# Optimization experiments

Measured on AMD Instinct MI355X. Metric: run time of the kernel, lower is better.

The kernel has to match this reference:

```python
import jax, jax.numpy as jnp
import numpy as np

B, N, H, D, L = 4, 1024, 8, 256, 4
SVD, NSP = 16, 512
DK = D // H
EPS = 1e-6


def setup_inputs() -> dict:
    key = jax.random.key(0)
    ks = jax.random.split(key, 40)
    p = {}
    p["x"] = jax.random.normal(ks[0], (B, N, D), jnp.float32)
    p["in_degrees"] = jax.random.randint(ks[1], (N,), 0, N)
    p["out_degrees"] = jax.random.randint(ks[2], (N,), 0, N)
    p["spatial_pos"] = jax.random.randint(ks[3], (N, N), 0, NSP)
    p["svd_emb"] = jax.random.normal(ks[4], (N, 2 * SVD), jnp.float32)
    # embedding tables (padding_idx=0 -> zero row)
    p["in_deg_emb"] = (0.02 * jax.random.normal(ks[5], (N, D), jnp.float32)).at[0].set(0.0)
    p["out_deg_emb"] = (0.02 * jax.random.normal(ks[6], (N, D), jnp.float32)).at[0].set(0.0)
    p["spatial_emb"] = (0.02 * jax.random.normal(ks[7], (NSP, H), jnp.float32)).at[0].set(0.0)
    # SVD linear (stored [in, out]; y = x @ W + b)
    p["W_svd"] = 0.02 * jax.random.normal(ks[8], (2 * SVD, D), jnp.float32)
    p["b_svd"] = jnp.zeros((D,), jnp.float32)
    # per-layer stacked transformer params
    names = ["Wq", "Wk", "Wv", "Wa", "W1", "W2"]
    for i, nm in enumerate(names):
        p[nm] = 0.05 * jax.random.normal(ks[9 + i], (L, D, D), jnp.float32)
    for nm in ["bq", "bk", "bv", "ba", "b1", "b2", "ln1_b", "ln2_b"]:
        p[nm] = jnp.zeros((L, D), jnp.float32)
    p["ln1_g"] = jnp.ones((L, D), jnp.float32)
    p["ln2_g"] = jnp.ones((L, D), jnp.float32)
    return p


def _ln(x, g, b):
    mu = jnp.mean(x, axis=-1, keepdims=True)
    var = jnp.mean(jnp.square(x - mu), axis=-1, keepdims=True)
    return (x - mu) * jax.lax.rsqrt(var + EPS) * g + b


def _forward(x, svd_emb, W_svd, b_svd, in_deg_emb, out_deg_emb, spatial_emb,
             Wq, bq, Wk, bk, Wv, bv, Wa, ba, ln1_g, ln1_b,
             W1, b1, W2, b2, ln2_g, ln2_b,
             in_degrees, out_degrees, spatial_pos):
    # node-level: degree embeddings ([N,D] broadcasts over batch)
    x = x + in_deg_emb[in_degrees] + out_deg_emb[out_degrees]
    # node-level: SVD embedding (deterministic sign = +1 -> concat(u, -v))
    pos = jnp.concatenate([svd_emb[:, :SVD], -svd_emb[:, SVD:]], axis=-1)
    x = x + pos @ W_svd + b_svd
    # attention-level spatial bias: [N,N,H] -> [H,N,N], broadcast over batch
    attn_bias = jnp.transpose(spatial_emb[spatial_pos], (2, 0, 1))
    scale = 1.0 / jnp.sqrt(jnp.asarray(DK, x.dtype))

    def body(h, params):
        wq, bq_, wk, bk_, wv, bv_, wa, ba_, g1, b1_, w1, bb1, w2, bb2, g2, b2_ = params
        q = (h @ wq + bq_).reshape(B, N, H, DK)
        k = (h @ wk + bk_).reshape(B, N, H, DK)
        v = (h @ wv + bv_).reshape(B, N, H, DK)
        # scores [B,H,N,N] + spatial bias [H,N,N]
        scores = jnp.einsum('bqhd,bkhd->bhqk', q, k) * scale + attn_bias
        attn = jax.nn.softmax(scores, axis=-1)
        o = jnp.einsum('bhqk,bkhd->bqhd', attn, v).reshape(B, N, D)
        h = _ln(h + o @ wa + ba_, g1, b1_)
        f = jnp.maximum(h @ w1 + bb1, 0.0) @ w2 + bb2
        h = _ln(h + f, g2, b2_)
        return h, None

    x, _ = jax.lax.scan(body, x, (Wq, bq, Wk, bk, Wv, bv, Wa, ba, ln1_g, ln1_b,
                                  W1, b1, W2, b2, ln2_g, ln2_b))
    return x


def reference(x, svd_emb, W_svd, b_svd, in_deg_emb, out_deg_emb, spatial_emb,
              Wq, bq, Wk, bk, Wv, bv, Wa, ba, ln1_g, ln1_b,
              W1, b1, W2, b2, ln2_g, ln2_b,
              in_degrees, out_degrees, spatial_pos):
    return _forward(x, svd_emb, W_svd, b_svd, in_deg_emb, out_deg_emb, spatial_emb,
                    Wq, bq, Wk, bk, Wv, bv, Wa, ba, ln1_g, ln1_b,
                    W1, b1, W2, b2, ln2_g, ln2_b,
                    in_degrees, out_degrees, spatial_pos)
```

## Files before the change

### kernel.cpp

```cpp
#include <hip/hip_runtime.h>
#include <hip/hip_bf16.h>
#include <math.h>

#define NN 1024
#define BB 4
#define HH 8
#define DD 256
#define LL 4
#define DKK 32
#define MM 4096
#define EPSF 1e-6f
#define LOG2EF 1.4426950408889634f
#define SCLOG2E 0.2550348625f

typedef __attribute__((ext_vector_type(8))) short short8;
typedef __attribute__((ext_vector_type(4))) float f32x4;
typedef unsigned int u32;

__device__ __forceinline__ unsigned short f2bf(float f) {
    __hip_bfloat16 h = __float2bfloat16(f);
    return *(unsigned short*)&h;
}
__device__ __forceinline__ float bf2f(unsigned short u) {
    unsigned v = ((unsigned)u) << 16;
    return __builtin_bit_cast(float, v);
}

__global__ __launch_bounds__(256) void init_kernel(
    const float* __restrict__ x, const int* __restrict__ deg_in,
    const int* __restrict__ deg_out, const float* __restrict__ svd,
    const float* __restrict__ in_emb, const float* __restrict__ out_emb,
    const float* __restrict__ Wsvd, const float* __restrict__ bsvd,
    const float* __restrict__ Wq, const float* __restrict__ Wk,
    const float* __restrict__ Wv, const float* __restrict__ Wa,
    const float* __restrict__ W1, const float* __restrict__ W2,
    const int* __restrict__ sp, const float* __restrict__ spemb,
    float* __restrict__ h, short* __restrict__ hb,
    short* __restrict__ Wt, short* __restrict__ bsw)
{
    int blk = blockIdx.x;
    int tid = threadIdx.x;
    {
        int n = blk & (NN - 1);
        int di = deg_in[n], dou = deg_out[n];
        float acc = x[(size_t)blk * DD + tid] + in_emb[(size_t)di * DD + tid]
                  + out_emb[(size_t)dou * DD + tid] + bsvd[tid];
        const float* sv = &svd[n * 32];
#pragma unroll
        for (int j = 0; j < 32; ++j) {
            float v = sv[j];
            v = (j < 16) ? v : -v;
            acc += v * Wsvd[j * DD + tid];
        }
        h[(size_t)blk * DD + tid] = acc;
        hb[(size_t)blk * DD + tid] = (short)f2bf(acc);
    }
    if (blk < 384) {
        __shared__ float t[64][65];
        int z = blk >> 4, tile = blk & 15;
        int name = z >> 2;
        const float* srcs[6] = {Wq, Wk, Wv, Wa, W1, W2};
        const float* W = srcs[name] + (size_t)(z & 3) * DD * DD;
        short* dst = Wt + (size_t)z * DD * DD;
        int r0 = (tile >> 2) * 64, c0 = (tile & 3) * 64;
#pragma unroll
        for (int i = 0; i < 16; ++i) {
            int idx = i * 256 + tid;
            int r = idx >> 6, cc = idx & 63;
            t[r][cc] = W[(size_t)(r0 + r) * DD + c0 + cc];
        }
        __syncthreads();
#pragma unroll
        for (int i = 0; i < 16; ++i) {
            int idx = i * 256 + tid;
            int n = idx >> 6, kk = idx & 63;
            dst[(size_t)(c0 + n) * DD + r0 + kk] = (short)f2bf(t[kk][n]);
        }
    } else if (blk < 1408) {
        int bb = blk - 384;
        int part = bb & 3;
        int tt = (bb >> 2) * 256 + tid;
        int ln = tt & 63, kt = (tt >> 6) & 15, q16 = tt >> 10;
        int qd = ln >> 4, cc = ln & 15;
        unsigned buf[8][2];
#pragma unroll
        for (int r = 0; r < 4; ++r) {
            int row = q16 * 16 + qd * 4 + r;
            int colj = kt * 64 + part * 16 + cc;
            int pp = sp[row * NN + colj];
            float4 e0 = *(const float4*)&spemb[pp * 8];
            float4 e1 = *(const float4*)&spemb[pp * 8 + 4];
            float ev[8] = {e0.x, e0.y, e0.z, e0.w, e1.x, e1.y, e1.z, e1.w};
#pragma unroll
            for (int hh = 0; hh < 8; ++hh) {
                unsigned short u = f2bf(ev[hh] * LOG2EF);
                if (r & 1) buf[hh][r >> 1] |= ((unsigned)u) << 16;
                else       buf[hh][r >> 1] = u;
            }
        }
#pragma unroll
        for (int hh = 0; hh < 8; ++hh) {
            uint2* dst = (uint2*)&bsw[(((size_t)hh * 64 + q16) * 16 + kt) * 1024
                                      + (size_t)ln * 16 + part * 4];
            *dst = make_uint2(buf[hh][0], buf[hh][1]);
        }
    }
}

__global__ __launch_bounds__(256) void gemm_qkv_kernel(
    const short* __restrict__ A,
    const short* __restrict__ Wtq, const short* __restrict__ Wtk,
    const short* __restrict__ Wtv,
    const float* __restrict__ bq, const float* __restrict__ bk,
    const float* __restrict__ bv,
    short* __restrict__ qo, short* __restrict__ ko, short* __restrict__ vo)
{
    int z = blockIdx.z;
    const short* Wt = (z == 0) ? Wtq : (z == 1) ? Wtk : Wtv;
    const float* bs = (z == 0) ? bq : (z == 1) ? bk : bv;
    int tid = threadIdx.x, wave = tid >> 6, lane = tid & 63;
    int quad = lane >> 4, c = lane & 15;
    int m0 = blockIdx.x * 16;
    int n0 = blockIdx.y * 64 + wave * 16;
    f32x4 acc = {0.f, 0.f, 0.f, 0.f};
    const short* Ap = &A[(size_t)(m0 + c) * DD];
#pragma unroll
    for (int ks = 0; ks < 8; ++ks) {
        short8 af = *(const short8*)&Ap[ks * 32 + quad * 8];
        short8 bf = *(const short8*)&Wt[(size_t)(n0 + c) * DD + ks * 32 + quad * 8];
        acc = __builtin_amdgcn_mfma_f32_16x16x32_bf16(af, bf, acc, 0, 0, 0);
    }
    int b = m0 >> 10;
    int tok0 = (m0 & (NN - 1)) + quad * 4;
    int col = n0 + c;
    int head = col >> 5, dk = col & 31;
    int bh = b * 8 + head;
    float bv2 = bs[col];
    if (z == 2) {
        ushort4 pk;
        pk.x = f2bf(acc[0] + bv2); pk.y = f2bf(acc[1] + bv2);
        pk.z = f2bf(acc[2] + bv2); pk.w = f2bf(acc[3] + bv2);
        *(ushort4*)&vo[((size_t)bh * DKK + dk) * NN + tok0] = pk;
    } else {
        short* out = (z == 0) ? qo : ko;
        float sc = (z == 0) ? SCLOG2E : 1.0f;
#pragma unroll
        for (int r = 0; r < 4; ++r)
            out[((size_t)bh * NN + tok0 + r) * DKK + dk] =
                (short)f2bf((acc[r] + bv2) * sc);
    }
}

__global__ __launch_bounds__(64) void attn_kernel(
    const short* __restrict__ q, const short* __restrict__ k,
    const short* __restrict__ vt, const short* __restrict__ bsw,
    short* __restrict__ obuf)
{
    int blk = blockIdx.x;
    int head = blk & 7;
    int rest = blk >> 3;
    int qt = rest & 63;
    int b = rest >> 6;
    int lane = threadIdx.x;
    int quad = lane >> 4, c = lane & 15;
    int bh = b * 8 + head;
    int q0 = qt * 16;
    int m0 = b * NN + q0;

    __shared__ short bl[16][1024];
    __shared__ short P[16][72];
    const f32x4 zero = {0.f, 0.f, 0.f, 0.f};

    const short* bbase = &bsw[(((size_t)head * 64 + qt) * 16) * 1024 + (size_t)lane * 16];
#pragma unroll
    for (int t = 0; t < 16; ++t) {
        __builtin_amdgcn_global_load_lds(
            (const __attribute__((address_space(1))) u32*)(bbase + (size_t)t * 1024),
            (__attribute__((address_space(3))) u32*)&bl[t][0], 16, 0, 0);
        __builtin_amdgcn_global_load_lds(
            (const __attribute__((address_space(1))) u32*)(bbase + (size_t)t * 1024 + 8),
            (__attribute__((address_space(3))) u32*)&bl[t][512], 16, 0, 0);
    }

    short8 qf = *(const short8*)&q[((size_t)bh * NN + q0 + c) * DKK + quad * 8];
    f32x4 Oa0 = zero, Oa1 = zero;
    float lsum[4] = {0.f, 0.f, 0.f, 0.f};

    short8 kf[4];
#pragma unroll
    for (int f = 0; f < 4; ++f)
        kf[f] = *(const short8*)&k[((size_t)bh * NN + f * 16 + c) * DKK + quad * 8];

    asm volatile("s_waitcnt vmcnt(0)" ::: "memory");
    __builtin_amdgcn_sched_barrier(0);

    for (int kti = 0; kti < 16; ++kti) {
        int kt = kti * 64;
        f32x4 s[4];
#pragma unroll
        for (int f = 0; f < 4; ++f)
            s[f] = __builtin_amdgcn_mfma_f32_16x16x32_bf16(qf, kf[f], zero, 0, 0, 0);
        if (kti < 15) {
#pragma unroll
            for (int f = 0; f < 4; ++f)
                kf[f] = *(const short8*)&k[((size_t)bh * NN + kt + 64 + f * 16 + c) * DKK + quad * 8];
        }
        short8 vf0[2], vf1[2];
#pragma unroll
        for (int kc = 0; kc < 2; ++kc) {
            vf0[kc] = *(const short8*)&vt[((size_t)bh * DKK + 0  + c) * NN + kt + kc * 32 + quad * 8];
            vf1[kc] = *(const short8*)&vt[((size_t)bh * DKK + 16 + c) * NN + kt + kc * 32 + quad * 8];
        }
        short8 bc0 = *(const short8*)&bl[kti][lane * 8];
        short8 bc1 = *(const short8*)&bl[kti][512 + lane * 8];
#pragma unroll
        for (int f = 0; f < 4; ++f)
#pragma unroll
            for (int r = 0; r < 4; ++r) {
                int jj = f * 4 + r;
                unsigned short uu = (unsigned short)((jj < 8) ? bc0[jj] : bc1[jj - 8]);
                float p = __builtin_amdgcn_exp2f(s[f][r] + bf2f(uu));
                s[f][r] = p;
                lsum[r] += p;
            }
#pragma unroll
        for (int f = 0; f < 4; ++f)
#pragma unroll
            for (int r = 0; r < 4; ++r)
                P[quad * 4 + r][f * 16 + c] = (short)f2bf(s[f][r]);
#pragma unroll
        for (int kc = 0; kc < 2; ++kc) {
            short8 pf = *(const short8*)&P[c][kc * 32 + quad * 8];
            Oa0 = __builtin_amdgcn_mfma_f32_16x16x32_bf16(pf, vf0[kc], Oa0, 0, 0, 0);
            Oa1 = __builtin_amdgcn_mfma_f32_16x16x32_bf16(pf, vf1[kc], Oa1, 0, 0, 0);
        }
    }
#pragma unroll
    for (int r = 0; r < 4; ++r)
#pragma unroll
        for (int off = 1; off < 16; off <<= 1)
            lsum[r] += __shfl_xor(lsum[r], off);
#pragma unroll
    for (int r = 0; r < 4; ++r) {
        float invl = 1.0f / lsum[r];
        int rr = quad * 4 + r;
        obuf[(size_t)(m0 + rr) * DD + head * 32 + c]      = (short)f2bf(Oa0[r] * invl);
        obuf[(size_t)(m0 + rr) * DD + head * 32 + 16 + c] = (short)f2bf(Oa1[r] * invl);
    }
}

template <int QKV>
__global__ __launch_bounds__(512) void post_kernel(
    const short* __restrict__ obuf,
    const short* __restrict__ Wta, const short* __restrict__ Wt1,
    const short* __restrict__ Wt2,
    const float* __restrict__ ba, const float* __restrict__ b1,
    const float* __restrict__ b2,
    const float* __restrict__ g1, const float* __restrict__ lb1,
    const float* __restrict__ g2, const float* __restrict__ lb2,
    float* __restrict__ h,
    const short* __restrict__ Wtqn, const short* __restrict__ Wtkn,
    const short* __restrict__ Wtvn,
    const float* __restrict__ bqn, const float* __restrict__ bkn,
    const float* __restrict__ bvn,
    short* __restrict__ qo, short* __restrict__ ko, short* __restrict__ vo)
{
    int tid = threadIdx.x, wave = tid >> 6, lane = tid & 63;
    int quad = lane >> 4, c = lane & 15;
    int m0 = blockIdx.x * 16;
    int b = m0 >> 10;
    int q0 = m0 & (NN - 1);
    int nb = wave * 32;

    __shared__ short t_in[16][264];
    __shared__ short t1s[16][264];
    __shared__ float shs[8][16][2];
    const f32x4 zero = {0.f, 0.f, 0.f, 0.f};

    {
        int row = tid >> 5, cg = tid & 31;
        *(short8*)&t_in[row][cg * 8] = *(const short8*)&obuf[(size_t)(m0 + row) * DD + cg * 8];
    }
    __syncthreads();

    f32x4 acc[2] = {zero, zero};
#pragma unroll
    for (int ks = 0; ks < 8; ++ks) {
        short8 af = *(const short8*)&t_in[c][ks * 32 + quad * 8];
#pragma unroll
        for (int f = 0; f < 2; ++f) {
            short8 bf = *(const short8*)&Wta[(size_t)(nb + f * 16 + c) * DD + ks * 32 + quad * 8];
            acc[f] = __builtin_amdgcn_mfma_f32_16x16x32_bf16(af, bf, acc[f], 0, 0, 0);
        }
    }
    float val[2][4];
    float ps[4] = {0.f,0.f,0.f,0.f}, ps2[4] = {0.f,0.f,0.f,0.f};
#pragma unroll
    for (int f = 0; f < 2; ++f) {
        int col = nb + f * 16 + c;
        float bv = ba[col];
#pragma unroll
        for (int r = 0; r < 4; ++r) {
            float v = h[(size_t)(m0 + quad * 4 + r) * DD + col] + acc[f][r] + bv;
            val[f][r] = v;
            ps[r] += v;
            ps2[r] += v * v;
        }
    }
#pragma unroll
    for (int r = 0; r < 4; ++r)
#pragma unroll
        for (int off = 1; off < 16; off <<= 1) {
            ps[r]  += __shfl_xor(ps[r], off);
            ps2[r] += __shfl_xor(ps2[r], off);
        }
    if (c == 0)
#pragma unroll
        for (int r = 0; r < 4; ++r) {
            shs[wave][quad * 4 + r][0] = ps[r];
            shs[wave][quad * 4 + r][1] = ps2[r];
        }
    __syncthreads();
    float res[2][4];
#pragma unroll
    for (int r = 0; r < 4; ++r) {
        int rr = quad * 4 + r;
        float ts = 0.f, t2 = 0.f;
#pragma unroll
        for (int w = 0; w < 8; ++w) { ts += shs[w][rr][0]; t2 += shs[w][rr][1]; }
        float mu = ts * (1.0f / DD);
        float rv = rsqrtf(t2 * (1.0f / DD) - mu * mu + EPSF);
#pragma unroll
        for (int f = 0; f < 2; ++f) {
            int col = nb + f * 16 + c;
            float nv = (val[f][r] - mu) * rv * g1[col] + lb1[col];
            res[f][r] = nv;
            t_in[rr][col] = (short)f2bf(nv);
        }
    }
    __syncthreads();
#pragma unroll
    for (int f = 0; f < 2; ++f) {
        int n0 = nb + f * 16;
        f32x4 a1 = zero;
#pragma unroll
        for (int ks = 0; ks < 8; ++ks) {
            short8 af = *(const short8*)&t_in[c][ks * 32 + quad * 8];
            short8 bf = *(const short8*)&Wt1[(size_t)(n0 + c) * DD + ks * 32 + quad * 8];
            a1 = __builtin_amdgcn_mfma_f32_16x16x32_bf16(af, bf, a1, 0, 0, 0);
        }
        float bv = b1[n0 + c];
#pragma unroll
        for (int r = 0; r < 4; ++r)
            t1s[quad * 4 + r][n0 + c] = (short)f2bf(fmaxf(a1[r] + bv, 0.f));
    }
    __syncthreads();
    f32x4 acc2[2] = {zero, zero};
#pragma unroll
    for (int ks = 0; ks < 8; ++ks) {
        short8 af = *(const short8*)&t1s[c][ks * 32 + quad * 8];
#pragma unroll
        for (int f = 0; f < 2; ++f) {
            short8 bf = *(const short8*)&Wt2[(size_t)(nb + f * 16 + c) * DD + ks * 32 + quad * 8];
            acc2[f] = __builtin_amdgcn_mfma_f32_16x16x32_bf16(af, bf, acc2[f], 0, 0, 0);
        }
    }
    float ps_2[4] = {0.f,0.f,0.f,0.f}, ps2_2[4] = {0.f,0.f,0.f,0.f};
#pragma unroll
    for (int f = 0; f < 2; ++f) {
        int col = nb + f * 16 + c;
        float bv = b2[col];
#pragma unroll
        for (int r = 0; r < 4; ++r) {
            float v = res[f][r] + acc2[f][r] + bv;
            val[f][r] = v;
            ps_2[r] += v;
            ps2_2[r] += v * v;
        }
    }
#pragma unroll
    for (int r = 0; r < 4; ++r)
#pragma unroll
        for (int off = 1; off < 16; off <<= 1) {
            ps_2[r]  += __shfl_xor(ps_2[r], off);
            ps2_2[r] += __shfl_xor(ps2_2[r], off);
        }
    __syncthreads();
    if (c == 0)
#pragma unroll
        for (int r = 0; r < 4; ++r) {
            shs[wave][quad * 4 + r][0] = ps_2[r];
            shs[wave][quad * 4 + r][1] = ps2_2[r];
        }
    __syncthreads();
#pragma unroll
    for (int r = 0; r < 4; ++r) {
        int rr = quad * 4 + r;
        float ts = 0.f, t2 = 0.f;
#pragma unroll
        for (int w = 0; w < 8; ++w) { ts += shs[w][rr][0]; t2 += shs[w][rr][1]; }
        float mu = ts * (1.0f / DD);
        float rv = rsqrtf(t2 * (1.0f / DD) - mu * mu + EPSF);
#pragma unroll
        for (int f = 0; f < 2; ++f) {
            int col = nb + f * 16 + c;
            float nv = (val[f][r] - mu) * rv * g2[col] + lb2[col];
            h[(size_t)(m0 + rr) * DD + col] = nv;
            t_in[rr][col] = (short)f2bf(nv);
        }
    }
    if (QKV == 0) return;
    __syncthreads();
    {
        int tok0 = q0 + quad * 4;
        const short* Wz[3] = {Wtqn, Wtkn, Wtvn};
        const float* bz[3] = {bqn, bkn, bvn};
#pragma unroll
        for (int z = 0; z < 3; ++z) {
#pragma unroll
            for (int f = 0; f < 2; ++f) {
                int n0 = nb + f * 16;
                f32x4 aq = zero;
#pragma unroll
                for (int ks = 0; ks < 8; ++ks) {
                    short8 af = *(const short8*)&t_in[c][ks * 32 + quad * 8];
                    short8 bf = *(const short8*)&Wz[z][(size_t)(n0 + c) * DD + ks * 32 + quad * 8];
                    aq = __builtin_amdgcn_mfma_f32_16x16x32_bf16(af, bf, aq, 0, 0, 0);
                }
                int col = n0 + c;
                int hd = col >> 5, dk = col & 31;
                int bh2 = b * 8 + hd;
                float bv2 = bz[z][col];
                if (z == 2) {
                    ushort4 pk;
                    pk.x = f2bf(aq[0] + bv2); pk.y = f2bf(aq[1] + bv2);
                    pk.z = f2bf(aq[2] + bv2); pk.w = f2bf(aq[3] + bv2);
                    *(ushort4*)&vo[((size_t)bh2 * DKK + dk) * NN + tok0] = pk;
                } else {
                    short* out = (z == 0) ? qo : ko;
                    float sc = (z == 0) ? SCLOG2E : 1.0f;
#pragma unroll
                    for (int r = 0; r < 4; ++r)
                        out[((size_t)bh2 * NN + tok0 + r) * DKK + dk] =
                            (short)f2bf((aq[r] + bv2) * sc);
                }
            }
        }
    }
}

extern "C" void kernel_launch(void* const* d_in, const int* in_sizes, int n_in,
                              void* d_out, int out_size, void* d_ws, size_t ws_size,
                              hipStream_t stream)
{
    const float* x       = (const float*)d_in[0];
    const int*   deg_in  = (const int*)d_in[1];
    const int*   deg_out = (const int*)d_in[2];
    const int*   sp      = (const int*)d_in[3];
    const float* svd     = (const float*)d_in[4];
    const float* in_emb  = (const float*)d_in[5];
    const float* out_emb = (const float*)d_in[6];
    const float* spemb   = (const float*)d_in[7];
    const float* Wsvd    = (const float*)d_in[8];
    const float* bsvd    = (const float*)d_in[9];
    const float* Wq = (const float*)d_in[10];
    const float* Wk = (const float*)d_in[11];
    const float* Wv = (const float*)d_in[12];
    const float* Wa = (const float*)d_in[13];
    const float* W1 = (const float*)d_in[14];
    const float* W2 = (const float*)d_in[15];
    const float* bq = (const float*)d_in[16];
    const float* bk = (const float*)d_in[17];
    const float* bv = (const float*)d_in[18];
    const float* ba = (const float*)d_in[19];
    const float* b1 = (const float*)d_in[20];
    const float* b2 = (const float*)d_in[21];
    const float* ln1b = (const float*)d_in[22];
    const float* ln2b = (const float*)d_in[23];
    const float* ln1g = (const float*)d_in[24];
    const float* ln2g = (const float*)d_in[25];

    float* h = (float*)d_out;
    char*  ws = (char*)d_ws;
    short* bias = (short*)ws;
    short* qb   = (short*)(ws + ((size_t)16 << 20));
    short* kb   = (short*)(ws + ((size_t)18 << 20));
    short* vtb  = (short*)(ws + ((size_t)20 << 20));
    short* obuf = (short*)(ws + ((size_t)22 << 20));
    short* hb   = (short*)(ws + ((size_t)26 << 20));
    short* Wt   = (short*)(ws + ((size_t)28 << 20));

    init_kernel<<<MM, 256, 0, stream>>>(x, deg_in, deg_out, svd, in_emb,
        out_emb, Wsvd, bsvd, Wq, Wk, Wv, Wa, W1, W2, sp, spemb, h, hb, Wt, bias);

    const size_t WSZ = (size_t)DD * DD;
    gemm_qkv_kernel<<<dim3(MM / 16, 4, 3), 256, 0, stream>>>(
        hb, Wt + 0 * WSZ, Wt + 4 * WSZ, Wt + 8 * WSZ, bq, bk, bv, qb, kb, vtb);

    for (int l = 0; l < LL; ++l) {
        const size_t bo = (size_t)l * DD;
        const short* Wta = Wt + (3 * 4 + l) * WSZ;
        const short* Wt1 = Wt + (4 * 4 + l) * WSZ;
        const short* Wt2 = Wt + (5 * 4 + l) * WSZ;

        attn_kernel<<<BB * HH * 64, 64, 0, stream>>>(qb, kb, vtb, bias, obuf);

        if (l < LL - 1) {
            const size_t bo_n = (size_t)(l + 1) * DD;
            post_kernel<1><<<MM / 16, 512, 0, stream>>>(
                obuf, Wta, Wt1, Wt2,
                ba + bo, b1 + bo, b2 + bo,
                ln1g + bo, ln1b + bo, ln2g + bo, ln2b + bo, h,
                Wt + (0 * 4 + l + 1) * WSZ, Wt + (1 * 4 + l + 1) * WSZ,
                Wt + (2 * 4 + l + 1) * WSZ,
                bq + bo_n, bk + bo_n, bv + bo_n, qb, kb, vtb);
        } else {
            post_kernel<0><<<MM / 16, 512, 0, stream>>>(
                obuf, Wta, Wt1, Wt2,
                ba + bo, b1 + bo, b2 + bo,
                ln1g + bo, ln1b + bo, ln2g + bo, ln2b + bo, h,
                nullptr, nullptr, nullptr, nullptr, nullptr, nullptr,
                nullptr, nullptr, nullptr);
        }
    }
}
```

Measured before the change: 364.2 us.

## Share K/V tiles across 8 waves via double-buffered LDS in attention

The attention kernel now runs 8 waves per block, each handling a different 16-query tile of the same batch-head. K and V tiles are staged cooperatively into double-buffered LDS with async global-to-LDS loads, so eight query tiles reuse one copy instead of each wave reloading from global memory. The per-wave spatial bias is no longer preloaded whole into LDS; it is instead register-prefetched one step ahead from global memory. The cost is a block-wide barrier every key tile and a grid that drops to 256 blocks, which may leave compute units underoccupied.

```diff
diff --git a/kernel.cpp b/kernel.cpp
--- a/kernel.cpp
+++ b/kernel.cpp
@@ -151,68 +151,78 @@
     }
 }
 
-__global__ __launch_bounds__(64) void attn_kernel(
+__global__ __launch_bounds__(512) void attn_kernel(
     const short* __restrict__ q, const short* __restrict__ k,
     const short* __restrict__ vt, const short* __restrict__ bsw,
     short* __restrict__ obuf)
 {
     int blk = blockIdx.x;
     int head = blk & 7;
-    int rest = blk >> 3;
-    int qt = rest & 63;
-    int b = rest >> 6;
-    int lane = threadIdx.x;
+    int b = (blk >> 3) & 3;
+    int qg = blk >> 5;
+    int tid = threadIdx.x, wave = tid >> 6, lane = tid & 63;
     int quad = lane >> 4, c = lane & 15;
     int bh = b * 8 + head;
+    int qt = qg * 8 + wave;
     int q0 = qt * 16;
     int m0 = b * NN + q0;
 
-    __shared__ short bl[16][1024];
-    __shared__ short P[16][72];
+    __shared__ short Ks[2][64][32];
+    __shared__ short Vs[2][32][64];
+    __shared__ short P[8][16][72];
     const f32x4 zero = {0.f, 0.f, 0.f, 0.f};
 
+    auto stage = [&](int t, int buf) {
+        if (wave < 4) {
+            const short* src = &k[((size_t)bh * NN + t * 64 + wave * 16 + (lane >> 2)) * DKK
+                                  + (lane & 3) * 8];
+            __builtin_amdgcn_global_load_lds(
+                (const __attribute__((address_space(1))) u32*)src,
+                (__attribute__((address_space(3))) u32*)&Ks[buf][wave * 16][0], 16, 0, 0);
+        } else {
+            const short* src = &vt[((size_t)bh * DKK + (wave - 4) * 8 + (lane >> 3)) * NN
+                                   + t * 64 + (lane & 7) * 8];
+            __builtin_amdgcn_global_load_lds(
+                (const __attribute__((address_space(1))) u32*)src,
+                (__attribute__((address_space(3))) u32*)&Vs[buf][(wave - 4) * 8][0], 16, 0, 0);
+        }
+    };
+
+    stage(0, 0);
+
+    short8 qf = *(const short8*)&q[((size_t)bh * NN + q0 + c) * DKK + quad * 8];
     const short* bbase = &bsw[(((size_t)head * 64 + qt) * 16) * 1024 + (size_t)lane * 16];
-#pragma unroll
-    for (int t = 0; t < 16; ++t) {
-        __builtin_amdgcn_global_load_lds(
-            (const __attribute__((address_space(1))) u32*)(bbase + (size_t)t * 1024),
-            (__attribute__((address_space(3))) u32*)&bl[t][0], 16, 0, 0);
-        __builtin_amdgcn_global_load_lds(
-            (const __attribute__((address_space(1))) u32*)(bbase + (size_t)t * 1024 + 8),
-            (__attribute__((address_space(3))) u32*)&bl[t][512], 16, 0, 0);
-    }
-
-    short8 qf = *(const short8*)&q[((size_t)bh * NN + q0 + c) * DKK + quad * 8];
+    short8 bc0 = *(const short8*)bbase;
+    short8 bc1 = *(const short8*)(bbase + 8);
+
     f32x4 Oa0 = zero, Oa1 = zero;
     float lsum[4] = {0.f, 0.f, 0.f, 0.f};
 
-    short8 kf[4];
-#pragma unroll
-    for (int f = 0; f < 4; ++f)
-        kf[f] = *(const short8*)&k[((size_t)bh * NN + f * 16 + c) * DKK + quad * 8];
-
-    asm volatile("s_waitcnt vmcnt(0)" ::: "memory");
-    __builtin_amdgcn_sched_barrier(0);
+    __syncthreads();
 
     for (int kti = 0; kti < 16; ++kti) {
-        int kt = kti * 64;
+        int cur = kti & 1;
+        if (kti < 15) stage(kti + 1, cur ^ 1);
+        short8 kf[4];
+#pragma unroll
+        for (int f = 0; f < 4; ++f)
+            kf[f] = *(const short8*)&Ks[cur][f * 16 + c][quad * 8];
+        short8 vf0[2], vf1[2];
+#pragma unroll
+        for (int kc = 0; kc < 2; ++kc) {
+            vf0[kc] = *(const short8*)&Vs[cur][c][kc * 32 + quad * 8];
+            vf1[kc] = *(const short8*)&Vs[cur][16 + c][kc * 32 + quad * 8];
+        }
         f32x4 s[4];
 #pragma unroll
         for (int f = 0; f < 4; ++f)
             s[f] = __builtin_amdgcn_mfma_f32_16x16x32_bf16(qf, kf[f], zero, 0, 0, 0);
+        short8 bn0 = bc0, bn1 = bc1;
         if (kti < 15) {
-#pragma unroll
-            for (int f = 0; f < 4; ++f)
-                kf[f] = *(const short8*)&k[((size_t)bh * NN + kt + 64 + f * 16 + c) * DKK + quad * 8];
-        }
-        short8 vf0[2], vf1[2];
-#pragma unroll
-        for (int kc = 0; kc < 2; ++kc) {
-            vf0[kc] = *(const short8*)&vt[((size_t)bh * DKK + 0  + c) * NN + kt + kc * 32 + quad * 8];
-            vf1[kc] = *(const short8*)&vt[((size_t)bh * DKK + 16 + c) * NN + kt + kc * 32 + quad * 8];
-        }
-        short8 bc0 = *(const short8*)&bl[kti][lane * 8];
-        short8 bc1 = *(const short8*)&bl[kti][512 + lane * 8];
+            const short* bp = bbase + (size_t)(kti + 1) * 1024;
+            bn0 = *(const short8*)bp;
+            bn1 = *(const short8*)(bp + 8);
+        }
 #pragma unroll
         for (int f = 0; f < 4; ++f)
 #pragma unroll
@@ -223,17 +233,19 @@
                 s[f][r] = p;
                 lsum[r] += p;
             }
+        bc0 = bn0; bc1 = bn1;
 #pragma unroll
         for (int f = 0; f < 4; ++f)
 #pragma unroll
             for (int r = 0; r < 4; ++r)
-                P[quad * 4 + r][f * 16 + c] = (short)f2bf(s[f][r]);
+                P[wave][quad * 4 + r][f * 16 + c] = (short)f2bf(s[f][r]);
 #pragma unroll
         for (int kc = 0; kc < 2; ++kc) {
-            short8 pf = *(const short8*)&P[c][kc * 32 + quad * 8];
+            short8 pf = *(const short8*)&P[wave][c][kc * 32 + quad * 8];
             Oa0 = __builtin_amdgcn_mfma_f32_16x16x32_bf16(pf, vf0[kc], Oa0, 0, 0, 0);
             Oa1 = __builtin_amdgcn_mfma_f32_16x16x32_bf16(pf, vf1[kc], Oa1, 0, 0, 0);
         }
+        __syncthreads();
     }
 #pragma unroll
     for (int r = 0; r < 4; ++r)
@@ -503,7 +515,7 @@
         const short* Wt1 = Wt + (4 * 4 + l) * WSZ;
         const short* Wt2 = Wt + (5 * 4 + l) * WSZ;
 
-        attn_kernel<<<BB * HH * 64, 64, 0, stream>>>(qb, kb, vtb, bias, obuf);
+        attn_kernel<<<256, 512, 0, stream>>>(qb, kb, vtb, bias, obuf);
 
         if (l < LL - 1) {
             const size_t bo_n = (size_t)(l + 1) * DD;
```

After: 336.9 us. -7.5%, faster.
